# Kernel tuning notes

Hardware: AMD Instinct MI355X
Metric: run time of the kernel (lower is better)

The kernel has to match this reference:

```python
import jax, jax.numpy as jnp
import numpy as np

N, E, CS = 8, 256, 8
L2, M2 = 2048, 1024
L1 = M2 * CS            # 8192 tokens at depth-1
M1 = 4096
LLAST = M1 * CS         # 32768 tokens at last layer
S = L2 + L1 + LLAST     # 43008
NUM_VOCAB = 16
RES = 64


def _mixed_values(key, n, L, M):
    # values in {1,3}, with exactly M positions per row set to the 'mixed' token 2
    k1, k2 = jax.random.split(key)
    base = jax.random.randint(k1, (n, L), 0, 2) * 2 + 1
    perms = jax.vmap(lambda k: jax.random.permutation(k, L))(jax.random.split(k2, n))
    mask = jnp.zeros((n, L), bool).at[jnp.arange(n)[:, None], perms[:, :M]].set(True)
    return jnp.where(mask, 2, base).astype(jnp.int32)


def setup_inputs() -> dict:
    key = jax.random.key(0)
    ks = jax.random.split(key, 16)
    v2 = _mixed_values(ks[0], N, L2, M2)
    v1 = _mixed_values(ks[1], N, L1, M1)
    vl = jax.random.randint(ks[2], (N, LLAST), 1, 4).astype(jnp.int32)
    value = jnp.concatenate([v2, v1, vl], axis=1)
    depth = jnp.concatenate([
        jnp.full((N, L2), 4, jnp.int32),
        jnp.full((N, L1), 5, jnp.int32),
        jnp.full((N, LLAST), 6, jnp.int32)], axis=1)
    pos = jax.random.randint(ks[3], (N, S, 3), 0, RES).astype(jnp.int32)
    x = jax.random.normal(ks[4], (N, L2 // CS, E), jnp.float32)
    s = 0.02
    return {
        'x': x, 'value': value, 'depth': depth, 'pos': pos,
        'W2': jax.random.normal(ks[5], (E, E, CS), jnp.float32) * s,
        'b2': jax.random.normal(ks[6], (E,), jnp.float32) * s,
        'W1': jax.random.normal(ks[7], (E, E, CS), jnp.float32) * s,
        'b1': jax.random.normal(ks[8], (E,), jnp.float32) * s,
        'W0': jax.random.normal(ks[9], (E, E, CS), jnp.float32) * s,
        'b0': jax.random.normal(ks[10], (E,), jnp.float32) * s,
        'emb': jax.random.normal(ks[11], (3, RES, E), jnp.float32) * s,
        'lin_w': jax.random.normal(ks[12], (E, NUM_VOCAB + 1), jnp.float32) * s,
        'lin_b': jax.random.normal(ks[13], (NUM_VOCAB + 1,), jnp.float32) * s,
    }


def _deconv(h, W, b):
    # ConvTranspose1d with kernel_size == stride == CS: each input token emits CS outputs
    n, t, e = h.shape
    cs = W.shape[2]
    return jnp.einsum('nti,iok->ntko', h, W).reshape(n, t * cs, e) + b


def _compact(y, mask, M):
    # per-row: rows of y where mask, packed to the front (stable), zero padded to M rows
    T = y.shape[1]
    if mask.shape[1] < T:
        mask = jnp.pad(mask, ((0, 0), (0, T - mask.shape[1])))
    else:
        mask = mask[:, :T]
    order = jnp.argsort(jnp.where(mask, 0, 1), axis=1, stable=True)
    g = jnp.take_along_axis(y, order[:, :M, None], axis=1)
    keep = jnp.arange(M)[None, :] < jnp.sum(mask, axis=1)[:, None]
    return jnp.where(keep[:, :, None], g, 0.0)


def reference(x, value, depth, pos, W2, b2, W1, b1, W0, b0, emb, lin_w, lin_b):
    max_depth = int(jnp.max(depth))
    len_1 = jnp.sum(depth == max_depth - 1, axis=1)
    len_2 = jnp.sum(depth == max_depth - 2, axis=1)
    L1_ = int(jnp.max(len_1)); L2_ = int(jnp.max(len_2))
    j2 = jnp.arange(L2_); j1 = jnp.arange(L1_)
    val_2 = jnp.where(j2[None, :] < len_2[:, None], value[:, :L2_], 0)
    idx1 = jnp.clip(len_2[:, None] + j1[None, :], 0, value.shape[1] - 1)
    val_1 = jnp.where(j1[None, :] < len_1[:, None], jnp.take_along_axis(value, idx1, axis=1), 0)
    mix_1 = jnp.sum(val_1 == 2, axis=1); mix_2 = jnp.sum(val_2 == 2, axis=1)
    M1_ = int(jnp.max(mix_1)); M2_ = int(jnp.max(mix_2))

    y_2 = _deconv(x, W2, b2)                 # [N, T''*cs, E]
    x_1 = _compact(y_2, val_2 == 2, M2_)     # gather mixed depth-2 positions
    y_1 = _deconv(x_1, W1, b1)
    x_0 = _compact(y_1, val_1 == 2, M1_)     # gather mixed depth-1 positions
    y_0 = _deconv(x_0, W0, b0)               # [N, M1_*cs, E]

    len_last = int(jnp.sum(depth[0] == max_depth))  # uniform across batch (torch slicing requires it)
    p = pos[:, -len_last:]                   # [N, len_last, 3]
    enc = emb[0][p[..., 0]] + emb[1][p[..., 1]] + emb[2][p[..., 2]]
    y_0 = y_0 + enc
    return y_0 @ lin_w + lin_b
```

## Files before the change

kernel.cpp:

```cpp
#include <hip/hip_runtime.h>
#include <cstdint>
#include <cstddef>

#define SEQ     43008
#define LASTOFF 10240
#define NV      17

typedef __bf16 bf16x8 __attribute__((ext_vector_type(8)));
typedef float  f32x4  __attribute__((ext_vector_type(4)));

typedef __attribute__((address_space(1))) const void gv_t;
typedef __attribute__((address_space(3))) void       lv_t;

__device__ __forceinline__ ushort f2bf(float f) {
    union { float f; unsigned u; } x; x.f = f;
    unsigned r = x.u + 0x7FFFu + ((x.u >> 16) & 1u);
    return (ushort)(r >> 16);
}
__device__ __forceinline__ float bf2f(ushort h) {
    union { unsigned u; float f; } x; x.u = ((unsigned)h) << 16;
    return x.f;
}

__device__ __forceinline__ void stage_tile_w(char* ldsbase, const ushort* src,
                                             int row0, int k0, int nch, int wv,
                                             int nwv, int lane)
{
    int sub  = lane >> 3;
    int col8 = (lane & 7) ^ sub;
    const ushort* g0 = src + (size_t)(row0 + sub) * 256 + k0 + (col8 << 3);
    for (int ch = wv; ch < nch; ch += nwv) {
        const ushort* g = g0 + ((size_t)(ch << 3)) * 256;
        __builtin_amdgcn_global_load_lds((gv_t*)g, (lv_t*)(ldsbase + (ch << 10)), 16, 0, 0);
    }
}

__device__ __forceinline__ bf16x8 frag64(const char* lds, int row, int kk, int lane) {
    int r = row + (lane & 15);
    int byte = (r << 7) + ((kk + ((lane >> 4) << 3)) << 1);
    byte ^= (r & 7) << 4;
    return *(const bf16x8*)(lds + byte);
}

__global__ __launch_bounds__(256) void prep_main(
    const float* __restrict__ x, const float* __restrict__ W2,
    const float* __restrict__ W1, const float* __restrict__ W0,
    const float* __restrict__ lin_w, const int* __restrict__ value,
    const float* __restrict__ emb, const float* __restrict__ b0,
    const float* __restrict__ lin_b,
    ushort* __restrict__ xb, ushort* __restrict__ Wb2T,
    ushort* __restrict__ W1n, ushort* __restrict__ W0n,
    int* __restrict__ dest2,
    int* __restrict__ packT, int* __restrict__ cnt1,
    float* __restrict__ embLp)
{
    __shared__ __align__(16) char sm[33792];
    const int b = blockIdx.x;
    const int tid = threadIdx.x;

    if (b < 192) {
        int s   = b >> 6;
        int rem = b & 63;
        int i0  = (rem >> 3) << 5;
        int o0  = (rem & 7) << 5;
        const float* W = (s == 0) ? W2 : ((s == 1) ? W1 : W0);
        float* tl = (float*)sm;
        #pragma unroll
        for (int q = 0; q < 8; ++q) {
            int fid = (q << 8) + tid;
            int ri  = fid >> 6;
            int f   = (fid & 63) << 2;
            float4 v = *(const float4*)(W + (size_t)(i0 + ri) * 2048 + o0 * 8 + f);
            int ol = f >> 3;
            int c0 = f & 7;
            tl[((c0 + 0) * 32 + ol) * 33 + ri] = v.x;
            tl[((c0 + 1) * 32 + ol) * 33 + ri] = v.y;
            tl[((c0 + 2) * 32 + ol) * 33 + ri] = v.z;
            tl[((c0 + 3) * 32 + ol) * 33 + ri] = v.w;
        }
        __syncthreads();
        int seg = tid & 3;
        if (s >= 1) {
            ushort* Wn = (s == 1) ? W1n : W0n;
            #pragma unroll
            for (int it = 0; it < 4; ++it) {
                int rk = (it << 6) + (tid >> 2);
                int c = rk >> 5, ii = rk & 31;
                ushort v8[8];
                #pragma unroll
                for (int u = 0; u < 8; ++u)
                    v8[u] = f2bf(tl[(c * 32 + (seg << 3) + u) * 33 + ii]);
                *(int4*)(Wn + (c << 16) + (i0 + ii) * 256 + o0 + (seg << 3)) =
                    *(const int4*)v8;
            }
        } else {
            #pragma unroll
            for (int it = 0; it < 4; ++it) {
                int rk = (it << 6) + (tid >> 2);
                int j  = ((rk >> 5) << 8) + o0 + (rk & 31);
                ushort v8[8];
                #pragma unroll
                for (int u = 0; u < 8; ++u)
                    v8[u] = f2bf(tl[rk * 33 + (seg << 3) + u]);
                *(int4*)(Wb2T + ((size_t)j << 8) + i0 + (seg << 3)) =
                    *(const int4*)v8;
            }
        }
    } else if (b < 448) {
        int i8 = (((b - 192) << 8) + tid) << 3;
        float4 a  = *(const float4*)(x + i8);
        float4 bb = *(const float4*)(x + i8 + 4);
        ushort v[8] = { f2bf(a.x), f2bf(a.y), f2bf(a.z), f2bf(a.w),
                        f2bf(bb.x), f2bf(bb.y), f2bf(bb.z), f2bf(bb.w) };
        *(int4*)(xb + i8) = *(const int4*)v;
    } else if (b < 456) {
        int n    = b - 448;
        int base = n * SEQ;
        int* dst = dest2 + n * 2048;
        int cnt = 0;
        int vloc[8];
        #pragma unroll
        for (int i = 0; i < 8; ++i) {
            vloc[i] = value[base + tid * 8 + i];
            cnt += (vloc[i] == 2);
        }
        int* s = (int*)sm;
        s[tid] = cnt;
        __syncthreads();
        for (int off = 1; off < 256; off <<= 1) {
            int v = (tid >= off) ? s[tid - off] : 0;
            __syncthreads();
            s[tid] += v;
            __syncthreads();
        }
        int run = s[tid] - cnt;
        #pragma unroll
        for (int i = 0; i < 8; ++i) {
            int d = -1;
            if (vloc[i] == 2 && run < 1024) { d = run; ++run; }
            dst[tid * 8 + i] = d;
        }
    } else if (b < 464) {
        int n    = b - 456;
        int base = n * SEQ + 2048;
        int (*s8)[8] = (int(*)[8])sm;
        int cnt8[8] = {0,0,0,0,0,0,0,0};
        int vloc[32];
        #pragma unroll
        for (int i = 0; i < 32; ++i) {
            vloc[i] = value[base + tid * 32 + i];
            cnt8[i & 7] += (vloc[i] == 2);
        }
        #pragma unroll
        for (int k = 0; k < 8; ++k) s8[tid][k] = cnt8[k];
        __syncthreads();
        for (int off = 1; off < 256; off <<= 1) {
            int v[8];
            #pragma unroll
            for (int k = 0; k < 8; ++k) v[k] = (tid >= off) ? s8[tid - off][k] : 0;
            __syncthreads();
            #pragma unroll
            for (int k = 0; k < 8; ++k) s8[tid][k] += v[k];
            __syncthreads();
        }
        int runK[8], runTot = 0;
        #pragma unroll
        for (int k = 0; k < 8; ++k) { runK[k] = s8[tid][k] - cnt8[k]; runTot += runK[k]; }
        #pragma unroll
        for (int i = 0; i < 32; ++i) {
            if (vloc[i] == 2) {
                int k  = i & 7;
                int tp = (tid * 32 + i) >> 3;
                packT[(((n << 3) + k) << 10) + runK[k]] = (runTot << 16) | tp;
                runK[k]++; runTot++;
            }
        }
        if (tid < 8) cnt1[(n << 3) + tid] = s8[255][tid];
    } else {
        int idx = b - 464;
        int jd  = idx >> 6;
        int p   = idx & 63;
        float* er = (float*)sm;
        float* ps = er + 256;
        float e = emb[jd * 16384 + p * 256 + tid];
        if (jd == 0) e += b0[tid];
        er[tid] = e;
        __syncthreads();
        if (tid < 136) {
            int v = tid >> 3, part = tid & 7;
            const float* lw = lin_w + v;
            float s = 0.f;
            int o0 = part << 5;
            #pragma unroll 8
            for (int o = o0; o < o0 + 32; ++o)
                s = fmaf(er[o], lw[o * NV], s);
            ps[tid] = s;
        }
        __syncthreads();
        if (tid < 20) {
            float acc = 0.f;
            if (tid < NV) {
                #pragma unroll
                for (int q = 0; q < 8; ++q) acc += ps[tid * 8 + q];
                if (jd == 0) acc += lin_b[tid];
            }
            embLp[jd * 1280 + p * 20 + tid] = acc;
        }
    }
}

__global__ __launch_bounds__(256) void g2h(
    const ushort* __restrict__ A, const ushort* __restrict__ BT,
    const float* __restrict__ bias, const int* __restrict__ dest,
    ushort* __restrict__ Xout,
    const ushort* __restrict__ W0n, const float* __restrict__ lin_w,
    const ushort* __restrict__ W1n, const float* __restrict__ b1,
    ushort* __restrict__ Hf, float* __restrict__ K1f)
{
    extern __shared__ __align__(16) char smem[];
    const int tid = threadIdx.x;
    const int lane = tid & 63, wv = tid >> 6;

    if (blockIdx.x < 256) {
        const int bx = blockIdx.x;
        const int r0 = (bx & 15) << 7;
        const int c0 = (bx >> 4) << 7;
        const int wm = (wv >> 1) << 6;
        const int wn = (wv & 1) << 6;

        f32x4 acc[4][4] = {};

        stage_tile_w(smem,         A,  r0, 0, 16, wv, 4, lane);
        stage_tile_w(smem + 16384, BT, c0, 0, 16, wv, 4, lane);
        __syncthreads();

        for (int kt = 0; kt < 4; ++kt) {
            char* cb = smem + ((kt & 1) << 15);
            if (kt < 3) {
                char* nb = smem + (((kt + 1) & 1) << 15);
                int k0n = (kt + 1) << 6;
                stage_tile_w(nb,         A,  r0, k0n, 16, wv, 4, lane);
                stage_tile_w(nb + 16384, BT, c0, k0n, 16, wv, 4, lane);
            }
            #pragma unroll
            for (int ks = 0; ks < 2; ++ks) {
                int kk = ks << 5;
                bf16x8 af[4], bfr[4];
                #pragma unroll
                for (int i = 0; i < 4; ++i) af[i]  = frag64(cb, wm + i * 16, kk, lane);
                #pragma unroll
                for (int i = 0; i < 4; ++i) bfr[i] = frag64(cb + 16384, wn + i * 16, kk, lane);
                #pragma unroll
                for (int mi = 0; mi < 4; ++mi)
                    #pragma unroll
                    for (int ni = 0; ni < 4; ++ni)
                        acc[mi][ni] = __builtin_amdgcn_mfma_f32_16x16x32_bf16(
                            af[mi], bfr[ni], acc[mi][ni], 0, 0, 0);
            }
            __syncthreads();
        }

        const int obase = c0 & 255;
        const int cdx   = c0 >> 8;
        float bv[4];
        #pragma unroll
        for (int ni = 0; ni < 4; ++ni)
            bv[ni] = bias[obase + wn + ni * 16 + (lane & 15)];

        ushort* Cs = (ushort*)smem;
        #pragma unroll
        for (int mi = 0; mi < 4; ++mi)
            #pragma unroll
            for (int ni = 0; ni < 4; ++ni)
                #pragma unroll
                for (int r = 0; r < 4; ++r) {
                    int row = wm + mi * 16 + ((lane >> 4) << 2) + r;
                    int col = wn + ni * 16 + (lane & 15);
                    Cs[row * 136 + col] = f2bf(acc[mi][ni][r] + bv[ni]);
                }
        __syncthreads();

        for (int p = 0; p < 8; ++p) {
            int row = p * 16 + (tid >> 4);
            int gr  = r0 + row;
            int n   = gr >> 8, t = gr & 255;
            int d   = dest[n * 2048 + t * 8 + cdx];
            if (d >= 0) {
                int4 v = *(const int4*)&Cs[row * 136 + ((tid & 15) << 3)];
                *(int4*)&Xout[(((size_t)n * 1024 + d) << 8) + obase + ((tid & 15) << 3)] = v;
            }
        }
        return;
    }

    const int idx = blockIdx.x - 256;
    const int cp  = idx >> 3, cf = idx & 7;

    ushort* Gs  = (ushort*)smem;
    char*   Bs  = smem + 16384;
    char*   lwA = smem + 49152;

    for (int j = tid; j < 4096; j += 256) ((int*)lwA)[j] = 0;
    __syncthreads();
    {
        int kt = tid >> 6, kq = tid & 63;
        const float* lsrc = lin_w + tid * NV;
        #pragma unroll
        for (int v = 0; v < NV; ++v) {
            int byte = (v << 7) + (kq << 1);
            byte ^= (v & 7) << 4;
            *(ushort*)(lwA + (kt << 12) + byte) = f2bf(lsrc[v]);
        }
    }
    __syncthreads();

    const ushort* W0c = W0n + ((size_t)cf << 16);
    f32x4 acc[2][16];
    {
        f32x4 z = {0.f, 0.f, 0.f, 0.f};
        #pragma unroll
        for (int mi = 0; mi < 2; ++mi)
            #pragma unroll
            for (int ni = 0; ni < 16; ++ni) acc[mi][ni] = z;
    }
    for (int kt = 0; kt < 4; ++kt) {
        stage_tile_w(Bs, W0c, 0, kt << 6, 32, wv, 4, lane);
        __syncthreads();
        #pragma unroll
        for (int ks = 0; ks < 2; ++ks) {
            int kk = ks << 5;
            bf16x8 a0 = frag64(lwA + (kt << 12), 0,  kk, lane);
            bf16x8 a1 = frag64(lwA + (kt << 12), 16, kk, lane);
            #pragma unroll
            for (int ni = 0; ni < 16; ++ni) {
                bf16x8 bfr = frag64(Bs, ni << 4, kk, lane);
                acc[0][ni] = __builtin_amdgcn_mfma_f32_16x16x32_bf16(a0, bfr, acc[0][ni], 0, 0, 0);
                acc[1][ni] = __builtin_amdgcn_mfma_f32_16x16x32_bf16(a1, bfr, acc[1][ni], 0, 0, 0);
            }
        }
        __syncthreads();
    }

    #pragma unroll
    for (int mi = 0; mi < 2; ++mi)
        #pragma unroll
        for (int ni = 0; ni < 16; ++ni)
            #pragma unroll
            for (int r = 0; r < 4; ++r) {
                int v = (mi << 4) + ((lane >> 4) << 2) + r;
                int o = (ni << 4) + (lane & 15);
                int byte = (v << 7) + ((o & 63) << 1);
                byte ^= (v & 7) << 4;
                *(ushort*)((char*)Gs + ((o >> 6) << 12) + byte) = f2bf(acc[mi][ni][r]);
            }
    __syncthreads();

    if (cp == 0) {
        float bo = b1[tid];
        int kt = tid >> 6, kq = tid & 63;
        float p[NV];
        #pragma unroll
        for (int v = 0; v < NV; ++v) {
            int byte = (v << 7) + (kq << 1);
            byte ^= (v & 7) << 4;
            p[v] = bo * bf2f(*(const ushort*)((const char*)Gs + (kt << 12) + byte));
        }
        #pragma unroll
        for (int off = 32; off >= 1; off >>= 1)
            #pragma unroll
            for (int v = 0; v < NV; ++v)
                p[v] += __shfl_xor(p[v], off);
        float* Ks = (float*)lwA;
        if (lane == 0)
            #pragma unroll
            for (int v = 0; v < NV; ++v) Ks[wv * NV + v] = p[v];
        __syncthreads();
        if (tid < NV)
            K1f[cf * NV + tid] = Ks[tid] + Ks[NV + tid] + Ks[2 * NV + tid] + Ks[3 * NV + tid];
        if (cf == 7 && tid >= 136 && tid < 144) K1f[tid] = 0.f;
        __syncthreads();
    }

    const ushort* Wb1 = W1n + ((size_t)cp << 16);
    {
        f32x4 z = {0.f, 0.f, 0.f, 0.f};
        #pragma unroll
        for (int mi = 0; mi < 2; ++mi)
            #pragma unroll
            for (int ni = 0; ni < 16; ++ni) acc[mi][ni] = z;
    }
    for (int kt = 0; kt < 4; ++kt) {
        stage_tile_w(Bs, Wb1, 0, kt << 6, 32, wv, 4, lane);
        __syncthreads();
        #pragma unroll
        for (int ks = 0; ks < 2; ++ks) {
            int kk = ks << 5;
            bf16x8 a0 = frag64((char*)Gs + (kt << 12), 0,  kk, lane);
            bf16x8 a1 = frag64((char*)Gs + (kt << 12), 16, kk, lane);
            #pragma unroll
            for (int ni = 0; ni < 16; ++ni) {
                bf16x8 bfr = frag64(Bs, ni << 4, kk, lane);
                acc[0][ni] = __builtin_amdgcn_mfma_f32_16x16x32_bf16(a0, bfr, acc[0][ni], 0, 0, 0);
                acc[1][ni] = __builtin_amdgcn_mfma_f32_16x16x32_bf16(a1, bfr, acc[1][ni], 0, 0, 0);
            }
        }
        __syncthreads();
    }

    #pragma unroll
    for (int mi = 0; mi < 2; ++mi)
        #pragma unroll
        for (int ni = 0; ni < 16; ++ni)
            #pragma unroll
            for (int r = 0; r < 4; ++r) {
                int v = (mi << 4) + ((lane >> 4) << 2) + r;
                if (v < NV) {
                    int i = (ni << 4) + (lane & 15);
                    Hf[cp * 36864 + (cf * NV + v) * 256 + i] = f2bf(acc[mi][ni][r]);
                }
            }
    if (cf == 7)
        for (int j = tid; j < 2048; j += 256)
            Hf[cp * 36864 + 136 * 256 + j] = 0;
}

__global__ __launch_bounds__(256) void fused_out(
    const ushort* __restrict__ X1, const ushort* __restrict__ Hf,
    const float* __restrict__ embLp, const float* __restrict__ K1f,
    const int* __restrict__ packT, const int* __restrict__ cnt1,
    const int* __restrict__ pos, float* __restrict__ out)
{
    extern __shared__ __align__(16) char smem[];

    const int tid  = threadIdx.x;
    const int lane = tid & 63, wv = tid >> 6;
    const int bb = blockIdx.x;
    const int n  = bb >> 3, cp = bb & 7;
    const int t0 = blockIdx.y << 6;
    const int cnt = cnt1[bb];
    if (t0 >= cnt) return;
    const int cntL = min(64, cnt - t0);

    const int sub  = lane >> 3;
    const int col8 = (lane & 7) ^ sub;
    const int* pbase = packT + (bb << 10);
    int Ta = pbase[t0 + (wv << 3) + sub] & 1023;
    int Tb = pbase[t0 + ((wv + 4) << 3) + sub] & 1023;
    const ushort* ga0 = X1 + ((size_t)((n << 10) + Ta) << 8) + (col8 << 3);
    const ushort* gb0 = X1 + ((size_t)((n << 10) + Tb) << 8) + (col8 << 3);

    float* embLs = (float*)(smem + 53248);
    for (int i = tid; i < 3840; i += 256) embLs[i] = embLp[i];
    float* K1s = (float*)(smem + 68608);
    if (tid < 144) K1s[tid] = K1f[tid];
    int* Ds = (int*)(smem + 69184);
    if (tid < 64) Ds[tid] = (pbase[t0 + tid] >> 16) & 4095;

    const ushort* Hb = Hf + cp * 36864;

    __builtin_amdgcn_global_load_lds((gv_t*)ga0, (lv_t*)(smem + (wv << 10)), 16, 0, 0);
    __builtin_amdgcn_global_load_lds((gv_t*)gb0, (lv_t*)(smem + ((wv + 4) << 10)), 16, 0, 0);
    stage_tile_w(smem + 8192, Hb, 0, 0, 18, wv, 4, lane);
    __syncthreads();

    f32x4 acc[9] = {};
    for (int kt = 0; kt < 4; ++kt) {
        char* cb = smem + (kt & 1) * 26624;
        if (kt < 3) {
            char* nb = smem + ((kt + 1) & 1) * 26624;
            int k0n = (kt + 1) << 6;
            __builtin_amdgcn_global_load_lds((gv_t*)(ga0 + k0n), (lv_t*)(nb + (wv << 10)), 16, 0, 0);
            __builtin_amdgcn_global_load_lds((gv_t*)(gb0 + k0n), (lv_t*)(nb + ((wv + 4) << 10)), 16, 0, 0);
            stage_tile_w(nb + 8192, Hb, 0, k0n, 18, wv, 4, lane);
        }
        #pragma unroll
        for (int ks = 0; ks < 2; ++ks) {
            int kk = ks << 5;
            bf16x8 af = frag64(cb, wv << 4, kk, lane);
            #pragma unroll
            for (int ni = 0; ni < 9; ++ni) {
                bf16x8 bfr = frag64(cb + 8192, ni << 4, kk, lane);
                acc[ni] = __builtin_amdgcn_mfma_f32_16x16x32_bf16(af, bfr, acc[ni], 0, 0, 0);
            }
        }
        __syncthreads();
    }

    float* Cs = (float*)smem;
    #pragma unroll
    for (int ni = 0; ni < 9; ++ni) {
        int col = (ni << 4) + (lane & 15);
        if (col < 136) {
            #pragma unroll
            for (int r = 0; r < 4; ++r) {
                int row = (wv << 4) + ((lane >> 4) << 2) + r;
                Cs[row * 136 + col] = acc[ni][r];
            }
        }
    }
    __syncthreads();

    #pragma unroll
    for (int rr = 0; rr < 2; ++rr) {
        int rl = tid * 2 + rr;
        int r  = rl >> 3, c = rl & 7;
        int prow = n * SEQ + LASTOFF + (Ds[r] << 3) + c;
        const int* pp = pos + 3 * prow;
        const float* e0 = embLs +        pp[0] * 20;
        const float* e1 = embLs + 1280 + pp[1] * 20;
        const float* e2 = embLs + 2560 + pp[2] * 20;
        const float* k1 = K1s + c * 17;
        float* cr = Cs + rl * 17;
        #pragma unroll
        for (int v4 = 0; v4 < 16; v4 += 4) {
            float4 a = *(const float4*)(e0 + v4);
            float4 bq = *(const float4*)(e1 + v4);
            float4 cq = *(const float4*)(e2 + v4);
            cr[v4 + 0] += a.x + bq.x + cq.x + k1[v4 + 0];
            cr[v4 + 1] += a.y + bq.y + cq.y + k1[v4 + 1];
            cr[v4 + 2] += a.z + bq.z + cq.z + k1[v4 + 2];
            cr[v4 + 3] += a.w + bq.w + cq.w + k1[v4 + 3];
        }
        cr[16] += e0[16] + e1[16] + e2[16] + k1[16];
    }
    __syncthreads();

    for (int i4 = tid; i4 < 2176; i4 += 256) {
        int r  = (i4 * 1928) >> 16;
        int fo = i4 - r * 34;
        if (r < cntL) {
            *(float4*)(out + ((size_t)((n << 12) + Ds[r])) * 136 + (fo << 2)) =
                *(const float4*)(Cs + r * 136 + (fo << 2));
        }
    }
}

extern "C" void kernel_launch(void* const* d_in, const int* in_sizes, int n_in,
                              void* d_out, int out_size, void* d_ws, size_t ws_size,
                              hipStream_t stream)
{
    (void)in_sizes; (void)n_in; (void)out_size; (void)ws_size;
    const float* x     = (const float*)d_in[0];
    const int*   value = (const int*)d_in[1];
    const int*   pos   = (const int*)d_in[3];
    const float* W2    = (const float*)d_in[4];
    const float* b2    = (const float*)d_in[5];
    const float* W1    = (const float*)d_in[6];
    const float* b1    = (const float*)d_in[7];
    const float* W0    = (const float*)d_in[8];
    const float* b0    = (const float*)d_in[9];
    const float* emb   = (const float*)d_in[10];
    const float* lin_w = (const float*)d_in[11];
    const float* lin_b = (const float*)d_in[12];
    float* out = (float*)d_out;

    char* ws = (char*)d_ws;
    ushort* Wb2T  = (ushort*)(ws);
    ushort* W0n   = (ushort*)(ws + 2097152);
    ushort* W1n   = (ushort*)(ws + 3145728);
    ushort* xb    = (ushort*)(ws + 4194304);
    int*    dest2 = (int*)   (ws + 5242880);
    int*    cnt1  = (int*)   (ws + 5308416);
    int*    packT = (int*)   (ws + 5308672);
    ushort* x1b   = (ushort*)(ws + 5570816);
    float*  embLp = (float*) (ws + 9838848);
    ushort* Hf    = (ushort*)(ws + 9854208);
    float*  K1f   = (float*) (ws + 10444032);

    prep_main<<<656, 256, 0, stream>>>(x, W2, W1, W0, lin_w, value,
                                       emb, b0, lin_b,
                                       xb, Wb2T, W1n, W0n, dest2, packT, cnt1, embLp);
    g2h<<<320, 256, 65536, stream>>>(xb, Wb2T, b2, dest2, x1b,
                                     W0n, lin_w, W1n, b1, Hf, K1f);
    fused_out<<<dim3(64, 16), 256, 69632, stream>>>(x1b, Hf, embLp, K1f,
                                                    packT, cnt1, pos, out);
}
```

Baseline: 63.45 us.

## Fuse three launches into one cooperative persistent kernel with grid syncs

Merges the prep, g2h and fused-output kernels into a single cooperative kernel that loops over virtual block indices and separates phases with grid.sync. The shared-memory layout of the output phase is compacted so every phase fits in 64 KB, allowing two blocks per CU. The aim is to remove inter-launch gaps and tail overhead. The cost is grid barriers, fewer resident blocks than the original 1024-block launch, and occupancy and device queries on the host every call, with the three-kernel path kept as a fallback.

```diff
diff --git a/kernel.cpp b/kernel.cpp
--- a/kernel.cpp
+++ b/kernel.cpp
@@ -1,6 +1,9 @@
 #include <hip/hip_runtime.h>
+#include <hip/hip_cooperative_groups.h>
 #include <cstdint>
 #include <cstddef>
+
+namespace cg = cooperative_groups;
 
 #define SEQ     43008
 #define LASTOFF 10240
@@ -42,22 +45,14 @@
     return *(const bf16x8*)(lds + byte);
 }
 
-__global__ __launch_bounds__(256) void prep_main(
-    const float* __restrict__ x, const float* __restrict__ W2,
-    const float* __restrict__ W1, const float* __restrict__ W0,
-    const float* __restrict__ lin_w, const int* __restrict__ value,
-    const float* __restrict__ emb, const float* __restrict__ b0,
-    const float* __restrict__ lin_b,
-    ushort* __restrict__ xb, ushort* __restrict__ Wb2T,
-    ushort* __restrict__ W1n, ushort* __restrict__ W0n,
-    int* __restrict__ dest2,
-    int* __restrict__ packT, int* __restrict__ cnt1,
-    float* __restrict__ embLp)
-{
-    __shared__ __align__(16) char sm[33792];
-    const int b = blockIdx.x;
-    const int tid = threadIdx.x;
-
+
+__device__ __forceinline__ void phase_prep(int b, char* sm, int tid,
+    const float* x, const float* W2, const float* W1, const float* W0,
+    const float* lin_w, const int* value, const float* emb,
+    const float* b0, const float* lin_b,
+    ushort* xb, ushort* Wb2T, ushort* W1n, ushort* W0n,
+    int* dest2, int* packT, int* cnt1, float* embLp)
+{
     if (b < 192) {
         int s   = b >> 6;
         int rem = b & 63;
@@ -209,29 +204,23 @@
     }
 }
 
-__global__ __launch_bounds__(256) void g2h(
-    const ushort* __restrict__ A, const ushort* __restrict__ BT,
-    const float* __restrict__ bias, const int* __restrict__ dest,
-    ushort* __restrict__ Xout,
-    const ushort* __restrict__ W0n, const float* __restrict__ lin_w,
-    const ushort* __restrict__ W1n, const float* __restrict__ b1,
-    ushort* __restrict__ Hf, float* __restrict__ K1f)
-{
-    extern __shared__ __align__(16) char smem[];
-    const int tid = threadIdx.x;
-    const int lane = tid & 63, wv = tid >> 6;
-
-    if (blockIdx.x < 256) {
-        const int bx = blockIdx.x;
-        const int r0 = (bx & 15) << 7;
-        const int c0 = (bx >> 4) << 7;
+__device__ __forceinline__ void phase_g2h(int vb, char* smem, int tid,
+    int lane, int wv,
+    const ushort* xb, const ushort* Wb2T, const float* b2,
+    const int* dest2, ushort* x1b,
+    const ushort* W0n, const float* lin_w, const ushort* W1n,
+    const float* b1, ushort* Hf, float* K1f)
+{
+    if (vb < 256) {
+        const int r0 = (vb & 15) << 7;
+        const int c0 = (vb >> 4) << 7;
         const int wm = (wv >> 1) << 6;
         const int wn = (wv & 1) << 6;
 
         f32x4 acc[4][4] = {};
 
-        stage_tile_w(smem,         A,  r0, 0, 16, wv, 4, lane);
-        stage_tile_w(smem + 16384, BT, c0, 0, 16, wv, 4, lane);
+        stage_tile_w(smem,         xb,   r0, 0, 16, wv, 4, lane);
+        stage_tile_w(smem + 16384, Wb2T, c0, 0, 16, wv, 4, lane);
         __syncthreads();
 
         for (int kt = 0; kt < 4; ++kt) {
@@ -239,8 +228,8 @@
             if (kt < 3) {
                 char* nb = smem + (((kt + 1) & 1) << 15);
                 int k0n = (kt + 1) << 6;
-                stage_tile_w(nb,         A,  r0, k0n, 16, wv, 4, lane);
-                stage_tile_w(nb + 16384, BT, c0, k0n, 16, wv, 4, lane);
+                stage_tile_w(nb,         xb,   r0, k0n, 16, wv, 4, lane);
+                stage_tile_w(nb + 16384, Wb2T, c0, k0n, 16, wv, 4, lane);
             }
             #pragma unroll
             for (int ks = 0; ks < 2; ++ks) {
@@ -265,7 +254,7 @@
         float bv[4];
         #pragma unroll
         for (int ni = 0; ni < 4; ++ni)
-            bv[ni] = bias[obase + wn + ni * 16 + (lane & 15)];
+            bv[ni] = b2[obase + wn + ni * 16 + (lane & 15)];
 
         ushort* Cs = (ushort*)smem;
         #pragma unroll
@@ -284,16 +273,16 @@
             int row = p * 16 + (tid >> 4);
             int gr  = r0 + row;
             int n   = gr >> 8, t = gr & 255;
-            int d   = dest[n * 2048 + t * 8 + cdx];
+            int d   = dest2[n * 2048 + t * 8 + cdx];
             if (d >= 0) {
                 int4 v = *(const int4*)&Cs[row * 136 + ((tid & 15) << 3)];
-                *(int4*)&Xout[(((size_t)n * 1024 + d) << 8) + obase + ((tid & 15) << 3)] = v;
+                *(int4*)&x1b[(((size_t)n * 1024 + d) << 8) + obase + ((tid & 15) << 3)] = v;
             }
         }
         return;
     }
 
-    const int idx = blockIdx.x - 256;
+    const int idx = vb - 256;
     const int cp  = idx >> 3, cf = idx & 7;
 
     ushort* Gs  = (ushort*)smem;
@@ -424,19 +413,15 @@
             Hf[cp * 36864 + 136 * 256 + j] = 0;
 }
 
-__global__ __launch_bounds__(256) void fused_out(
-    const ushort* __restrict__ X1, const ushort* __restrict__ Hf,
-    const float* __restrict__ embLp, const float* __restrict__ K1f,
-    const int* __restrict__ packT, const int* __restrict__ cnt1,
-    const int* __restrict__ pos, float* __restrict__ out)
-{
-    extern __shared__ __align__(16) char smem[];
-
-    const int tid  = threadIdx.x;
-    const int lane = tid & 63, wv = tid >> 6;
-    const int bb = blockIdx.x;
+__device__ __forceinline__ void phase_fused(int vb, char* smem, int tid,
+    int lane, int wv,
+    const ushort* x1b, const ushort* Hf, const float* embLp,
+    const float* K1f, const int* packT, const int* cnt1,
+    const int* pos, float* out)
+{
+    const int bb = vb & 63;
     const int n  = bb >> 3, cp = bb & 7;
-    const int t0 = blockIdx.y << 6;
+    const int t0 = (vb >> 6) << 6;
     const int cnt = cnt1[bb];
     if (t0 >= cnt) return;
     const int cntL = min(64, cnt - t0);
@@ -446,15 +431,8 @@
     const int* pbase = packT + (bb << 10);
     int Ta = pbase[t0 + (wv << 3) + sub] & 1023;
     int Tb = pbase[t0 + ((wv + 4) << 3) + sub] & 1023;
-    const ushort* ga0 = X1 + ((size_t)((n << 10) + Ta) << 8) + (col8 << 3);
-    const ushort* gb0 = X1 + ((size_t)((n << 10) + Tb) << 8) + (col8 << 3);
-
-    float* embLs = (float*)(smem + 53248);
-    for (int i = tid; i < 3840; i += 256) embLs[i] = embLp[i];
-    float* K1s = (float*)(smem + 68608);
-    if (tid < 144) K1s[tid] = K1f[tid];
-    int* Ds = (int*)(smem + 69184);
-    if (tid < 64) Ds[tid] = (pbase[t0 + tid] >> 16) & 4095;
+    const ushort* ga0 = x1b + ((size_t)((n << 10) + Ta) << 8) + (col8 << 3);
+    const ushort* gb0 = x1b + ((size_t)((n << 10) + Tb) << 8) + (col8 << 3);
 
     const ushort* Hb = Hf + cp * 36864;
 
@@ -498,6 +476,12 @@
             }
         }
     }
+    float* embLs = (float*)(smem + 36864);
+    for (int i = tid; i < 3840; i += 256) embLs[i] = embLp[i];
+    float* K1s = (float*)(smem + 52224);
+    if (tid < 144) K1s[tid] = K1f[tid];
+    int* Ds = (int*)(smem + 52800);
+    if (tid < 64) Ds[tid] = (pbase[t0 + tid] >> 16) & 4095;
     __syncthreads();
 
     #pragma unroll
@@ -533,6 +517,81 @@
                 *(const float4*)(Cs + r * 136 + (fo << 2));
         }
     }
+}
+
+__global__ __launch_bounds__(256, 2) void mega(
+    const float* __restrict__ x, const float* __restrict__ W2,
+    const float* __restrict__ W1, const float* __restrict__ W0,
+    const float* __restrict__ lin_w, const int* __restrict__ value,
+    const float* __restrict__ emb, const float* __restrict__ b0,
+    const float* __restrict__ lin_b, const float* __restrict__ b1,
+    const float* __restrict__ b2, const int* __restrict__ pos,
+    ushort* __restrict__ xb, ushort* __restrict__ Wb2T,
+    ushort* __restrict__ W1n, ushort* __restrict__ W0n,
+    int* __restrict__ dest2, int* __restrict__ packT,
+    int* __restrict__ cnt1, float* __restrict__ embLp,
+    ushort* __restrict__ x1b, ushort* __restrict__ Hf,
+    float* __restrict__ K1f, float* __restrict__ out)
+{
+    extern __shared__ __align__(16) char smem[];
+    cg::grid_group grid = cg::this_grid();
+    const int tid  = threadIdx.x;
+    const int lane = tid & 63, wv = tid >> 6;
+
+    for (int b = blockIdx.x; b < 656; b += gridDim.x) {
+        __syncthreads();
+        phase_prep(b, smem, tid, x, W2, W1, W0, lin_w, value, emb, b0, lin_b,
+                   xb, Wb2T, W1n, W0n, dest2, packT, cnt1, embLp);
+    }
+    __threadfence();
+    grid.sync();
+
+    for (int vb = blockIdx.x; vb < 320; vb += gridDim.x) {
+        __syncthreads();
+        phase_g2h(vb, smem, tid, lane, wv, xb, Wb2T, b2, dest2, x1b,
+                  W0n, lin_w, W1n, b1, Hf, K1f);
+    }
+    __threadfence();
+    grid.sync();
+
+    for (int vb = blockIdx.x; vb < 1024; vb += gridDim.x) {
+        __syncthreads();
+        phase_fused(vb, smem, tid, lane, wv, x1b, Hf, embLp, K1f,
+                    packT, cnt1, pos, out);
+    }
+}
+
+__global__ __launch_bounds__(256) void prep_k(
+    const float* x, const float* W2, const float* W1, const float* W0,
+    const float* lin_w, const int* value, const float* emb,
+    const float* b0, const float* lin_b,
+    ushort* xb, ushort* Wb2T, ushort* W1n, ushort* W0n,
+    int* dest2, int* packT, int* cnt1, float* embLp)
+{
+    __shared__ __align__(16) char sm[33792];
+    phase_prep(blockIdx.x, sm, threadIdx.x, x, W2, W1, W0, lin_w, value, emb,
+               b0, lin_b, xb, Wb2T, W1n, W0n, dest2, packT, cnt1, embLp);
+}
+
+__global__ __launch_bounds__(256) void g2h_k(
+    const ushort* xb, const ushort* Wb2T, const float* b2,
+    const int* dest2, ushort* x1b,
+    const ushort* W0n, const float* lin_w, const ushort* W1n,
+    const float* b1, ushort* Hf, float* K1f)
+{
+    extern __shared__ __align__(16) char smem[];
+    phase_g2h(blockIdx.x, smem, threadIdx.x, threadIdx.x & 63, threadIdx.x >> 6,
+              xb, Wb2T, b2, dest2, x1b, W0n, lin_w, W1n, b1, Hf, K1f);
+}
+
+__global__ __launch_bounds__(256) void fused_k(
+    const ushort* x1b, const ushort* Hf, const float* embLp,
+    const float* K1f, const int* packT, const int* cnt1,
+    const int* pos, float* out)
+{
+    extern __shared__ __align__(16) char smem[];
+    phase_fused(blockIdx.x, smem, threadIdx.x, threadIdx.x & 63, threadIdx.x >> 6,
+                x1b, Hf, embLp, K1f, packT, cnt1, pos, out);
 }
 
 extern "C" void kernel_launch(void* const* d_in, const int* in_sizes, int n_in,
@@ -567,11 +626,39 @@
     ushort* Hf    = (ushort*)(ws + 9854208);
     float*  K1f   = (float*) (ws + 10444032);
 
-    prep_main<<<656, 256, 0, stream>>>(x, W2, W1, W0, lin_w, value,
-                                       emb, b0, lin_b,
-                                       xb, Wb2T, W1n, W0n, dest2, packT, cnt1, embLp);
-    g2h<<<320, 256, 65536, stream>>>(xb, Wb2T, b2, dest2, x1b,
-                                     W0n, lin_w, W1n, b1, Hf, K1f);
-    fused_out<<<dim3(64, 16), 256, 69632, stream>>>(x1b, Hf, embLp, K1f,
-                                                    packT, cnt1, pos, out);
-}
+    bool launched = false;
+    int nb = 0, ncu = 0, dev = 0;
+    hipError_t e0 = hipGetDevice(&dev);
+    hipError_t e1 = hipDeviceGetAttribute(&ncu, hipDeviceAttributeMultiprocessorCount, dev);
+    hipError_t e2 = hipOccupancyMaxActiveBlocksPerMultiprocessor(
+        &nb, (const void*)mega, 256, (size_t)65536);
+    if (e0 == hipSuccess && e1 == hipSuccess && e2 == hipSuccess &&
+        nb >= 1 && ncu >= 1) {
+        long cap = (long)nb * (long)ncu;
+        int grid = (int)(cap < 512 ? cap : 512);
+        void* args[] = {
+            (void*)&x, (void*)&W2, (void*)&W1, (void*)&W0, (void*)&lin_w,
+            (void*)&value, (void*)&emb, (void*)&b0, (void*)&lin_b, (void*)&b1,
+            (void*)&b2, (void*)&pos,
+            (void*)&xb, (void*)&Wb2T, (void*)&W1n, (void*)&W0n,
+            (void*)&dest2, (void*)&packT, (void*)&cnt1, (void*)&embLp,
+            (void*)&x1b, (void*)&Hf, (void*)&K1f, (void*)&out
+        };
+        hipError_t le = hipLaunchCooperativeKernel((const void*)mega, dim3(grid),
+                                                   dim3(256), args, 65536, stream);
+        if (le == hipSuccess) launched = true;
+        else (void)hipGetLastError();
+    } else {
+        (void)hipGetLastError();
+    }
+
+    if (!launched) {
+        prep_k<<<656, 256, 0, stream>>>(x, W2, W1, W0, lin_w, value, emb,
+                                        b0, lin_b, xb, Wb2T, W1n, W0n,
+                                        dest2, packT, cnt1, embLp);
+        g2h_k<<<320, 256, 65536, stream>>>(xb, Wb2T, b2, dest2, x1b,
+                                           W0n, lin_w, W1n, b1, Hf, K1f);
+        fused_k<<<1024, 256, 65536, stream>>>(x1b, Hf, embLp, K1f,
+                                              packT, cnt1, pos, out);
+    }
+}
```

Result: slower. 237.1 us (+273.7%).
